# Performance work log

Measured on AMD Instinct MI355X. Metric: run time of the kernel, lower is better.

The kernel has to match this reference:

```python
import jax, jax.numpy as jnp
import numpy as np

HIDDEN = 1024
HEADS = 16
HEAD_DIM = HIDDEN // HEADS


def setup_inputs() -> dict:
    key = jax.random.key(0)
    ks = jax.random.split(key, 7)
    B, S = 2, 2048
    scale = 1.0 / np.sqrt(HIDDEN)
    return {
        "hidden_states": jax.random.normal(ks[0], (B, S, HIDDEN), dtype=jnp.float32),
        "attention_mask": jnp.zeros((B, S), dtype=jnp.float32),
        "Wq": jax.random.normal(ks[1], (HIDDEN, HIDDEN), dtype=jnp.float32) * scale,
        "bq": jnp.zeros((HIDDEN,), dtype=jnp.float32),
        "Wk": jax.random.normal(ks[2], (HIDDEN, HIDDEN), dtype=jnp.float32) * scale,
        "bk": jnp.zeros((HIDDEN,), dtype=jnp.float32),
        "Wv": jax.random.normal(ks[3], (HIDDEN, HIDDEN), dtype=jnp.float32) * scale,
        "bv": jnp.zeros((HIDDEN,), dtype=jnp.float32),
    }


def reference(hidden_states, attention_mask, Wq, bq, Wk, bk, Wv, bv):
    B, S, _ = hidden_states.shape
    def heads(x):  # [B,S,HIDDEN] -> [B,H,S,D]
        return x.reshape(B, S, HEADS, HEAD_DIM).transpose(0, 2, 1, 3)
    q = heads(hidden_states @ Wq + bq)
    k = heads(hidden_states @ Wk + bk)
    v = heads(hidden_states @ Wv + bv)
    scores = jnp.einsum('bhqd,bhkd->bhqk', q, k) / np.sqrt(HEAD_DIM).astype(np.float32)
    # additive mask broadcast [B,1,1,S]
    scores = scores + attention_mask[:, None, None, :]
    probs = jax.nn.softmax(scores, axis=-1)
    # dropout is identity in eval mode (reference baseline)
    ctx = jnp.einsum('bhqk,bhkd->bhqd', probs, v)
    return ctx.transpose(0, 2, 1, 3).reshape(B, S, HIDDEN)
```

## Files before the change

### kernel.cpp

```cpp
#include <hip/hip_runtime.h>
#include <cstdint>
#include <cstddef>

typedef __bf16 bf16;
typedef __attribute__((ext_vector_type(8))) __bf16 bf16x8;
typedef __attribute__((ext_vector_type(4))) float f32x4;
typedef __attribute__((ext_vector_type(16))) float f32x16;
typedef __attribute__((ext_vector_type(4))) short short4v;

#define MFMA16(a, b, c) __builtin_amdgcn_mfma_f32_16x16x32_bf16((a), (b), (c), 0, 0, 0)
#define MFMA32(a, b, c) __builtin_amdgcn_mfma_f32_32x32x16_bf16((a), (b), (c), 0, 0, 0)

static constexpr int BB   = 2;
static constexpr int SS   = 2048;
static constexpr int HID  = 1024;
static constexpr int NH   = 16;
static constexpr int HD   = 64;
static constexpr int MROW = BB * SS;
static constexpr int NQKV = 3 * HID;
static constexpr float LOG2E = 1.4426950408889634f;
static constexpr float MSHIFT = 16.0f;

__device__ __forceinline__ int SW(int r) { return ((r ^ (r >> 3)) & 7) << 4; }

__device__ __forceinline__ uint32_t pack_bf16(float a, float b) {
    union { bf16 h[2]; uint32_t u; } x;
    x.h[0] = (bf16)a; x.h[1] = (bf16)b;
    return x.u;
}

__device__ __forceinline__ float exp2i(float x) {
    float r; asm("v_exp_f32 %0, %1" : "=v"(r) : "v"(x)); return r;
}

__device__ __forceinline__ void plswap(uint32_t& a, uint32_t& b) {
    asm("v_permlane32_swap_b32 %0, %1" : "+v"(a), "+v"(b));
}

__device__ __forceinline__ void gload16(const void* g, void* l) {
    __builtin_amdgcn_global_load_lds(
        (const __attribute__((address_space(1))) void*)g,
        (__attribute__((address_space(3))) void*)l, 16, 0, 0);
}

__global__ __launch_bounds__(256) void cvt_hidden(const float* __restrict__ in,
                                                  bf16* __restrict__ out) {
    const int i = (blockIdx.x * 256 + threadIdx.x) * 8;
    float4 f0 = *(const float4*)&in[i];
    float4 f1 = *(const float4*)&in[i + 4];
    bf16x8 o;
    o[0] = (bf16)f0.x; o[1] = (bf16)f0.y; o[2] = (bf16)f0.z; o[3] = (bf16)f0.w;
    o[4] = (bf16)f1.x; o[5] = (bf16)f1.y; o[6] = (bf16)f1.z; o[7] = (bf16)f1.w;
    *(bf16x8*)&out[i] = o;
}

__global__ __launch_bounds__(256) void maskcvt(const float* __restrict__ m,
                                               float* __restrict__ o) {
    const int i = blockIdx.x * 256 + threadIdx.x;
    o[i] = m[i] * LOG2E - MSHIFT;
}

__global__ __launch_bounds__(256) void wtrans(const float* __restrict__ Wq,
                                              const float* __restrict__ Wk,
                                              const float* __restrict__ Wv,
                                              bf16* __restrict__ Wt) {
    __shared__ float tile[32][33];
    const float* W = (blockIdx.z == 0) ? Wq : (blockIdx.z == 1) ? Wk : Wv;
    bf16* O = Wt + (size_t)blockIdx.z * HID * HID;
    const int x  = blockIdx.x * 32 + threadIdx.x;
    const int y0 = blockIdx.y * 32;
#pragma unroll
    for (int i = threadIdx.y; i < 32; i += 8)
        tile[i][threadIdx.x] = W[(size_t)(y0 + i) * HID + x];
    __syncthreads();
    const int k = y0 + threadIdx.x;
#pragma unroll
    for (int i = threadIdx.y; i < 32; i += 8)
        O[(size_t)(blockIdx.x * 32 + i) * HID + k] = (bf16)tile[threadIdx.x][i];
}

__global__ __launch_bounds__(256) void qkv_gemm(
    const bf16* __restrict__ A, const bf16* __restrict__ Bt,
    const float* __restrict__ bq, const float* __restrict__ bk,
    const float* __restrict__ bv,
    bf16* __restrict__ Qo, bf16* __restrict__ Ko, bf16* __restrict__ Vo) {
    __shared__ __align__(16) bf16 As[128 * 32];
    __shared__ __align__(16) bf16 Bs[128 * 32];
    const int t = threadIdx.x, l = t & 63;
    const int l15 = l & 15, l4 = l >> 4;
    const int w = t >> 6;
    const int wm = w >> 1, wn = w & 1;

    const int bid = blockIdx.x;
    const int nid = (bid & 7) * 96 + (bid >> 3);
    const int m0 = (nid & 31) * 128;
    const int n0 = (nid >> 5) * 128;

    f32x4 acc[4][4] = {};

    for (int kt = 0; kt < 32; ++kt) {
        const int k0 = kt * 32;
        __syncthreads();
#pragma unroll
        for (int cc = 0; cc < 2; ++cc) {
            const int c = t + cc * 256;
            const int row = c >> 2, col = (c & 3) * 8;
            gload16(&A[(size_t)(m0 + row) * HID + k0 + col], (char*)As + c * 16);
            gload16(&Bt[(size_t)(n0 + row) * HID + k0 + col], (char*)Bs + c * 16);
        }
        __syncthreads();

        bf16x8 af[4], bf_[4];
#pragma unroll
        for (int mi = 0; mi < 4; ++mi) {
            const int r = wm * 64 + mi * 16 + l15;
            af[mi] = *(const bf16x8*)((const char*)As + r * 64 + l4 * 16);
        }
#pragma unroll
        for (int ni = 0; ni < 4; ++ni) {
            const int r = wn * 64 + ni * 16 + l15;
            bf_[ni] = *(const bf16x8*)((const char*)Bs + r * 64 + l4 * 16);
        }
        __builtin_amdgcn_s_setprio(1);
#pragma unroll
        for (int mi = 0; mi < 4; ++mi)
#pragma unroll
            for (int ni = 0; ni < 4; ++ni)
                acc[mi][ni] = MFMA16(af[mi], bf_[ni], acc[mi][ni]);
        __builtin_amdgcn_s_setprio(0);
    }

#pragma unroll
    for (int mi = 0; mi < 4; ++mi) {
#pragma unroll
        for (int ni = 0; ni < 4; ++ni) {
            const int ng = n0 + wn * 64 + ni * 16 + l15;
            const int qkv = ng >> 10;
            const int nn = ng & 1023;
            const int hh = nn >> 6, dd = nn & 63;
            const int mg = m0 + wm * 64 + mi * 16 + l4 * 4;
            const int bb = mg >> 11, ss = mg & 2047;
            if (qkv == 2) {
                const float bias = bv[nn];
                union { bf16 h[4]; short4v s4; } pk_;
#pragma unroll
                for (int j = 0; j < 4; ++j)
                    pk_.h[j] = (bf16)(acc[mi][ni][j] + bias);
                bf16* dst = Vo + ((size_t)(bb * NH + hh) * HD + dd) * SS + ss;
                *(short4v*)dst = pk_.s4;
            } else {
                const float* bp = (qkv == 0) ? bq : bk;
                bf16* op = (qkv == 0) ? Qo : Ko;
                const float bias = bp[nn];
                const float scl = (qkv == 0) ? 0.125f * LOG2E : 1.0f;
                bf16* dst = op + ((size_t)(bb * NH + hh) * SS + ss) * HD + dd;
#pragma unroll
                for (int j = 0; j < 4; ++j)
                    dst[(size_t)j * HD] = (bf16)((acc[mi][ni][j] + bias) * scl);
            }
        }
    }
}

__global__ __launch_bounds__(256) void attn_fwd(
    const bf16* __restrict__ Q, const bf16* __restrict__ K,
    const bf16* __restrict__ Vt_g, const float* __restrict__ mkl,
    float* __restrict__ out) {
    __shared__ __align__(16) char smem[32768];

    const int t = threadIdx.x, l = t & 63, w = t >> 6;
    const int l31 = l & 31, h = l >> 5;

    const int bid = blockIdx.x;
    const int nid = (bid & 7) * 64 + (bid >> 3);
    const int bh = nid >> 4, qb = nid & 15;
    const int b = bh >> 4, hh = bh & 15;
    const int q0 = qb * 128 + w * 32;

    const bf16* Qp  = Q + (size_t)bh * SS * HD;
    const bf16* Kp  = K + (size_t)bh * SS * HD;
    const bf16* Vpt = Vt_g + (size_t)bh * HD * SS;
    const float* mkp = mkl + b * SS;

    bf16x8 qf[4];
#pragma unroll
    for (int c = 0; c < 4; ++c)
        qf[c] = *(const bf16x8*)&Qp[(size_t)(q0 + l31) * HD + c * 16 + h * 8];

    float lrun = 0.f;
    f32x16 o0 = {}, o1 = {};

    auto stageK = [&](int tile, char* dst) {
        const int key0 = tile * 64;
#pragma unroll
        for (int cc = 0; cc < 2; ++cc) {
            const int c = t + cc * 256;
            const int row = c >> 3;
            const int csw = (c & 7) ^ ((row ^ (row >> 3)) & 7);
            gload16(&Kp[(size_t)(key0 + row) * HD + csw * 8], dst + c * 16);
        }
    };
    auto stageVt = [&](int tile, char* dst) {
        const int key0 = tile * 64;
#pragma unroll
        for (int cc = 0; cc < 2; ++cc) {
            const int c = t + cc * 256;
            const int row = c >> 3;
            const int csw = (c & 7) ^ ((row ^ (row >> 3)) & 7);
            gload16(&Vpt[(size_t)row * SS + key0 + csw * 8], dst + c * 16);
        }
    };

    stageK(0, smem);
    stageVt(0, smem + 16384);
    __syncthreads();

    constexpr int NT = SS / 64;
#pragma unroll 1
    for (int kt = 0; kt < NT; ++kt) {
        char* Ks  = smem + (kt & 1) * 8192;
        char* Vt  = smem + 16384 + (kt & 1) * 8192;
        char* Ksn = smem + ((kt + 1) & 1) * 8192;
        char* Vtn = smem + 16384 + ((kt + 1) & 1) * 8192;
        const int key0 = kt * 64;
        const bool more = (kt + 1) < NT;

        if (more) {
            stageK(kt + 1, Ksn);
            stageVt(kt + 1, Vtn);
        }

        f32x16 s0, s1;
#pragma unroll
        for (int rq = 0; rq < 4; ++rq) {
            const f32x4 m0v = *(const f32x4*)&mkp[key0 + rq * 8 + 4 * h];
            const f32x4 m1v = *(const f32x4*)&mkp[key0 + 32 + rq * 8 + 4 * h];
#pragma unroll
            for (int j = 0; j < 4; ++j) {
                s0[rq * 4 + j] = m0v[j];
                s1[rq * 4 + j] = m1v[j];
            }
        }
        __builtin_amdgcn_s_setprio(1);
#pragma unroll
        for (int c = 0; c < 4; ++c) {
            const int r0 = l31;
            bf16x8 kf0 = *(const bf16x8*)(Ks + r0 * 128 +
                                          ((c * 32 + h * 16) ^ SW(r0)));
            s0 = MFMA32(kf0, qf[c], s0);
        }
#pragma unroll
        for (int c = 0; c < 4; ++c) {
            const int r1 = 32 + l31;
            bf16x8 kf1 = *(const bf16x8*)(Ks + r1 * 128 +
                                          ((c * 32 + h * 16) ^ SW(r1)));
            s1 = MFMA32(kf1, qf[c], s1);
        }
        __builtin_amdgcn_s_setprio(0);

#pragma unroll
        for (int g = 0; g < 2; ++g) {
            f32x16& st = g ? s1 : s0;
            float ps = 0.f;
#pragma unroll
            for (int r = 0; r < 16; ++r) {
                const float p = exp2i(st[r]);
                st[r] = p;
                ps += p;
            }
            lrun += ps;
#pragma unroll
            for (int cc = 0; cc < 2; ++cc) {
                uint32_t wA = pack_bf16(st[8 * cc + 0], st[8 * cc + 1]);
                uint32_t wB = pack_bf16(st[8 * cc + 2], st[8 * cc + 3]);
                uint32_t wC = pack_bf16(st[8 * cc + 4], st[8 * cc + 5]);
                uint32_t wD = pack_bf16(st[8 * cc + 6], st[8 * cc + 7]);
                plswap(wA, wC);
                plswap(wB, wD);
                union { uint32_t u[4]; bf16x8 v; } pb;
                pb.u[0] = wA; pb.u[1] = wB; pb.u[2] = wC; pb.u[3] = wD;
                const int colb = g * 64 + cc * 32 + h * 16;
                __builtin_amdgcn_s_setprio(1);
                {
                    bf16x8 vf0 = *(const bf16x8*)(Vt + l31 * 128 +
                                                  (colb ^ SW(l31)));
                    o0 = MFMA32(vf0, pb.v, o0);
                    const int r1 = 32 + l31;
                    bf16x8 vf1 = *(const bf16x8*)(Vt + r1 * 128 +
                                                  (colb ^ SW(r1)));
                    o1 = MFMA32(vf1, pb.v, o1);
                }
                __builtin_amdgcn_s_setprio(0);
            }
        }
        __syncthreads();
    }

    lrun += __shfl_xor(lrun, 32);
    const float inv = 1.0f / lrun;
    char* myB = smem + w * 8192;
#pragma unroll
    for (int r4 = 0; r4 < 4; ++r4) {
        f32x4 a, b2;
#pragma unroll
        for (int j = 0; j < 4; ++j) {
            a[j]  = o0[r4 * 4 + j] * inv;
            b2[j] = o1[r4 * 4 + j] * inv;
        }
        const int s0_ = 2 * r4 + h;
        const int s1_ = 8 + 2 * r4 + h;
        *(f32x4*)(myB + l31 * 256 + ((s0_ ^ (l31 & 15)) * 16)) = a;
        *(f32x4*)(myB + l31 * 256 + ((s1_ ^ (l31 & 15)) * 16)) = b2;
    }
    const int qr = l >> 1, halfd = l & 1;
    float* op = &out[((size_t)(b * SS) + q0 + qr) * HID + hh * HD + halfd * 32];
#pragma unroll
    for (int s = 0; s < 8; ++s) {
        const int slot = halfd * 8 + s;
        f32x4 v = *(const f32x4*)(myB + qr * 256 + ((slot ^ (qr & 15)) * 16));
        *(f32x4*)(op + s * 4) = v;
    }
}

extern "C" void kernel_launch(void* const* d_in, const int* in_sizes, int n_in,
                              void* d_out, int out_size, void* d_ws, size_t ws_size,
                              hipStream_t stream) {
    (void)in_sizes; (void)n_in; (void)out_size; (void)ws_size;
    const float* hs  = (const float*)d_in[0];
    const float* msk = (const float*)d_in[1];
    const float* Wq  = (const float*)d_in[2];
    const float* bq  = (const float*)d_in[3];
    const float* Wk  = (const float*)d_in[4];
    const float* bk  = (const float*)d_in[5];
    const float* Wv  = (const float*)d_in[6];
    const float* bv  = (const float*)d_in[7];
    float* out = (float*)d_out;
    char* ws = (char*)d_ws;
    const size_t MB = 1 << 20;

    bf16* Qb  = (bf16*)ws;
    bf16* Kb  = (bf16*)(ws + 8 * MB);
    bf16* Vb  = (bf16*)(ws + 16 * MB);
    float* mk2 = (float*)(ws + 24 * MB);
    bf16* Xb  = (bf16*)(ws + 25 * MB);
    bf16* Wt  = (bf16*)(ws + 33 * MB);

    cvt_hidden<<<dim3(MROW * HID / (256 * 8)), dim3(256), 0, stream>>>(hs, Xb);
    maskcvt<<<dim3(BB * SS / 256), dim3(256), 0, stream>>>(msk, mk2);
    wtrans<<<dim3(32, 32, 3), dim3(32, 8), 0, stream>>>(Wq, Wk, Wv, Wt);
    qkv_gemm<<<dim3(768), dim3(256), 0, stream>>>(
        Xb, Wt, bq, bk, bv, Qb, Kb, Vb);
    attn_fwd<<<dim3(512), dim3(256), 0, stream>>>(Qb, Kb, Vb, mk2, out);
}
```

Before: 114.7 us.

## Double-buffer QKV GEMM LDS tiles and fold mask conversion into cvt kernel

The QKV GEMM now ping-pongs between two LDS buffers and prefetches the next K-slice with global_load_lds while the MFMAs run on the current one. This replaces two barriers per iteration with one, so load latency can overlap compute. The mask conversion kernel is merged into the hidden-state conversion launch as extra blocks, removing one launch. Attention shared memory is split into four named arrays instead of one offset buffer, which may change how the compiler places LDS but adds no new logic. Doubling LDS use in the GEMM raises its footprint and may lower occupancy.

```diff
diff --git a/kernel.cpp b/kernel.cpp
--- a/kernel.cpp
+++ b/kernel.cpp
@@ -44,20 +44,22 @@
 }
 
 __global__ __launch_bounds__(256) void cvt_hidden(const float* __restrict__ in,
-                                                  bf16* __restrict__ out) {
-    const int i = (blockIdx.x * 256 + threadIdx.x) * 8;
+                                                  bf16* __restrict__ out,
+                                                  const float* __restrict__ msk,
+                                                  float* __restrict__ mk2) {
+    const int blk = blockIdx.x;
+    if (blk >= 2048) {
+        const int i = (blk - 2048) * 256 + threadIdx.x;
+        mk2[i] = msk[i] * LOG2E - MSHIFT;
+        return;
+    }
+    const int i = (blk * 256 + threadIdx.x) * 8;
     float4 f0 = *(const float4*)&in[i];
     float4 f1 = *(const float4*)&in[i + 4];
     bf16x8 o;
     o[0] = (bf16)f0.x; o[1] = (bf16)f0.y; o[2] = (bf16)f0.z; o[3] = (bf16)f0.w;
     o[4] = (bf16)f1.x; o[5] = (bf16)f1.y; o[6] = (bf16)f1.z; o[7] = (bf16)f1.w;
     *(bf16x8*)&out[i] = o;
-}
-
-__global__ __launch_bounds__(256) void maskcvt(const float* __restrict__ m,
-                                               float* __restrict__ o) {
-    const int i = blockIdx.x * 256 + threadIdx.x;
-    o[i] = m[i] * LOG2E - MSHIFT;
 }
 
 __global__ __launch_bounds__(256) void wtrans(const float* __restrict__ Wq,
@@ -84,8 +86,10 @@
     const float* __restrict__ bq, const float* __restrict__ bk,
     const float* __restrict__ bv,
     bf16* __restrict__ Qo, bf16* __restrict__ Ko, bf16* __restrict__ Vo) {
-    __shared__ __align__(16) bf16 As[128 * 32];
-    __shared__ __align__(16) bf16 Bs[128 * 32];
+    __shared__ __align__(16) bf16 As0[128 * 32];
+    __shared__ __align__(16) bf16 As1[128 * 32];
+    __shared__ __align__(16) bf16 Bs0[128 * 32];
+    __shared__ __align__(16) bf16 Bs1[128 * 32];
     const int t = threadIdx.x, l = t & 63;
     const int l15 = l & 15, l4 = l >> 4;
     const int w = t >> 6;
@@ -98,17 +102,25 @@
 
     f32x4 acc[4][4] = {};
 
-    for (int kt = 0; kt < 32; ++kt) {
+    auto stage = [&](int kt, bf16* Asd, bf16* Bsd) {
         const int k0 = kt * 32;
-        __syncthreads();
 #pragma unroll
         for (int cc = 0; cc < 2; ++cc) {
             const int c = t + cc * 256;
             const int row = c >> 2, col = (c & 3) * 8;
-            gload16(&A[(size_t)(m0 + row) * HID + k0 + col], (char*)As + c * 16);
-            gload16(&Bt[(size_t)(n0 + row) * HID + k0 + col], (char*)Bs + c * 16);
-        }
-        __syncthreads();
+            gload16(&A[(size_t)(m0 + row) * HID + k0 + col], (char*)Asd + c * 16);
+            gload16(&Bt[(size_t)(n0 + row) * HID + k0 + col], (char*)Bsd + c * 16);
+        }
+    };
+
+    stage(0, As0, Bs0);
+    __syncthreads();
+
+#pragma unroll 1
+    for (int kt = 0; kt < 32; ++kt) {
+        bf16* As = (kt & 1) ? As1 : As0;
+        bf16* Bs = (kt & 1) ? Bs1 : Bs0;
+        if (kt < 31) stage(kt + 1, (kt & 1) ? As0 : As1, (kt & 1) ? Bs0 : Bs1);
 
         bf16x8 af[4], bf_[4];
 #pragma unroll
@@ -128,6 +140,7 @@
             for (int ni = 0; ni < 4; ++ni)
                 acc[mi][ni] = MFMA16(af[mi], bf_[ni], acc[mi][ni]);
         __builtin_amdgcn_s_setprio(0);
+        __syncthreads();
     }
 
 #pragma unroll
@@ -166,7 +179,10 @@
     const bf16* __restrict__ Q, const bf16* __restrict__ K,
     const bf16* __restrict__ Vt_g, const float* __restrict__ mkl,
     float* __restrict__ out) {
-    __shared__ __align__(16) char smem[32768];
+    __shared__ __align__(16) char Ks0[64 * 128];
+    __shared__ __align__(16) char Ks1[64 * 128];
+    __shared__ __align__(16) char Vt0[64 * 128];
+    __shared__ __align__(16) char Vt1[64 * 128];
 
     const int t = threadIdx.x, l = t & 63, w = t >> 6;
     const int l31 = l & 31, h = l >> 5;
@@ -211,17 +227,17 @@
         }
     };
 
-    stageK(0, smem);
-    stageVt(0, smem + 16384);
+    stageK(0, Ks0);
+    stageVt(0, Vt0);
     __syncthreads();
 
     constexpr int NT = SS / 64;
 #pragma unroll 1
     for (int kt = 0; kt < NT; ++kt) {
-        char* Ks  = smem + (kt & 1) * 8192;
-        char* Vt  = smem + 16384 + (kt & 1) * 8192;
-        char* Ksn = smem + ((kt + 1) & 1) * 8192;
-        char* Vtn = smem + 16384 + ((kt + 1) & 1) * 8192;
+        char* Ks  = (kt & 1) ? Ks1 : Ks0;
+        char* Vt  = (kt & 1) ? Vt1 : Vt0;
+        char* Ksn = (kt & 1) ? Ks0 : Ks1;
+        char* Vtn = (kt & 1) ? Vt0 : Vt1;
         const int key0 = kt * 64;
         const bool more = (kt + 1) < NT;
 
@@ -298,7 +314,7 @@
 
     lrun += __shfl_xor(lrun, 32);
     const float inv = 1.0f / lrun;
-    char* myB = smem + w * 8192;
+    char* myB = (w == 0) ? Ks0 : (w == 1) ? Ks1 : (w == 2) ? Vt0 : Vt1;
 #pragma unroll
     for (int r4 = 0; r4 < 4; ++r4) {
         f32x4 a, b2;
@@ -345,8 +361,7 @@
     bf16* Xb  = (bf16*)(ws + 25 * MB);
     bf16* Wt  = (bf16*)(ws + 33 * MB);
 
-    cvt_hidden<<<dim3(MROW * HID / (256 * 8)), dim3(256), 0, stream>>>(hs, Xb);
-    maskcvt<<<dim3(BB * SS / 256), dim3(256), 0, stream>>>(msk, mk2);
+    cvt_hidden<<<dim3(2048 + 16), dim3(256), 0, stream>>>(hs, Xb, msk, mk2);
     wtrans<<<dim3(32, 32, 3), dim3(32, 8), 0, stream>>>(Wq, Wk, Wv, Wt);
     qkv_gemm<<<dim3(768), dim3(256), 0, stream>>>(
         Xb, Wt, bq, bk, bv, Qb, Kb, Vb);
```

Result: faster. 110.7 us (-3.4%).
